# Performance work log

Hardware: AMD Instinct MI355X
Metric: run time of the kernel (lower is better)

Reference implementation:

```python
import jax, jax.numpy as jnp
import numpy as np

B = 4096      # batch of states
N = 32        # SVGD particles per state
D_ACT = 16    # action dim
D_OBS = 64    # obs dim
H = 256       # critic hidden width
STEPS = 3     # num_svgd_steps
LR = 0.1      # svgd_lr
LIMIT = 1.0   # act_limit


def q_mlp(obs, x, w1, b1, w2, b2, w3, b3):
    # SAC-style critic: q(obs, a) -> scalar per row. obs/x: [BN, *]
    h = jnp.concatenate([obs, x], axis=-1)
    h = jax.nn.relu(h @ w1 + b1)
    h = jax.nn.relu(h @ w2 + b2)
    return (h @ w3 + b3)[..., 0]  # [BN]


def rbf_kernel(X, Y):
    # X: [B, N, D] (differentiable), Y: [B, N, D] (detached copy of X)
    diff = X[:, :, None, :] - Y[:, None, :, :]          # [B, N, N, D]
    dist_sq = jnp.sum(diff * diff, axis=-1)             # [B, N, N]
    # median heuristic bandwidth per batch element
    med = jnp.median(dist_sq.reshape(dist_sq.shape[0], -1), axis=-1)
    h = med / np.log(N) + 1e-8
    gamma = jax.lax.stop_gradient(1.0 / (2.0 * h))      # [B]
    K = jnp.exp(-gamma[:, None, None] * dist_sq)        # [B, N, N]
    # dK/dX (grad wrt first argument)
    K_grad = -2.0 * gamma[:, None, None, None] * diff * K[..., None]  # [B,N,N,D]
    return K, diff, gamma, K_grad


def setup_inputs() -> dict:
    key = jax.random.key(0)
    ks = jax.random.split(key, 6)
    BN = B * N
    sc = lambda k, shp: jax.random.normal(k, shp, jnp.float32) * 0.05
    return {
        "obs": jax.random.normal(ks[0], (BN, D_OBS), jnp.float32),
        "a": jax.random.normal(ks[1], (BN, D_ACT), jnp.float32),
        "w1": sc(ks[2], (D_OBS + D_ACT, H)),
        "b1": jnp.zeros((H,), jnp.float32),
        "w2": sc(ks[3], (H, H)),
        "b2": jnp.zeros((H,), jnp.float32),
        "w3": sc(ks[4], (H, 1)),
        "b3": jnp.zeros((1,), jnp.float32),
    }


def reference(obs, a, w1, b1, w2, b2, w3, b3):
    # a0 arrives detached in the original (sampler(obs, a0.detach(), ...))
    a = jax.lax.stop_gradient(a)
    logp = jnp.zeros((B, N), jnp.float32)
    q_fn = lambda X: q_mlp(obs, X, w1, b1, w2, b2, w3, b3)
    q_vals = None
    for _ in range(STEPS):
        # log_prob = min(q1, q1) == q1; score = d(sum q)/dX via vjp
        q_vals, vjp_fn = jax.vjp(q_fn, a)                 # q_vals: [BN]
        score, = vjp_fn(jnp.ones_like(q_vals))            # [BN, D_ACT]
        X = a.reshape(B, N, D_ACT)
        S = score.reshape(B, N, D_ACT)
        K, diff, gamma, K_grad = rbf_kernel(X, jax.lax.stop_gradient(X))
        # phi = (K.detach() @ score - K_grad.sum(2)) / N
        drive = jnp.einsum('bij,bjd->bid', jax.lax.stop_gradient(K), S)
        phi = (drive - K_grad.sum(axis=2)) / N            # [B, N, D]
        # logp correction terms
        tmp1 = (K_grad * S[:, None, :, :]).sum(-1).mean(-1)                 # [B, N]
        tmp2 = -2.0 * gamma[:, None] * (((-K_grad) * diff).sum(-1)
                                        - D_ACT * K).mean(-1)               # [B, N]
        logp = logp - LR * (tmp1 + tmp2)
        # svgd_optim + clamp + detach
        a = a + LR * phi.reshape(B * N, D_ACT)
        a = jax.lax.stop_gradient(jnp.clip(a, -LIMIT, LIMIT))
    return a.reshape(B, N, D_ACT), logp, q_vals
```

## Files before the change

kernel.cpp:

```cpp
#include <hip/hip_runtime.h>
#include <hip/hip_bf16.h>
#include <math.h>

#define BNROWS (4096*32)
#define RB     64
#define LN32   3.4657359027997265f

typedef __attribute__((ext_vector_type(8))) short bf16x8;
typedef __attribute__((ext_vector_type(4))) float f32x4;

static __device__ __forceinline__ ushort f2bf(float x) {
    union { __hip_bfloat16 h; ushort u; } cv;
    cv.h = __float2bfloat16(x);
    return cv.u;
}

__global__ void obs_to_bf16(const float* __restrict__ obs,
                            ushort* __restrict__ obs_bf) {
    size_t i = ((size_t)blockIdx.x * 256 + threadIdx.x) * 4;
    float4 v = *(const float4*)&obs[i];
    ushort4 o;
    o.x = f2bf(v.x); o.y = f2bf(v.y); o.z = f2bf(v.z); o.w = f2bf(v.w);
    *(ushort4*)&obs_bf[i] = o;
}

__global__ void prep_pack(const float* __restrict__ w1,
                          const float* __restrict__ w2,
                          ushort* __restrict__ pB1, ushort* __restrict__ pB2,
                          ushort* __restrict__ pB3, ushort* __restrict__ pB4) {
    int g = blockIdx.x * 256 + threadIdx.x;
    ushort out[8];
    ushort* dst;
    if (g < 3072) {
        int lane = g & 63, gc = g >> 6;
        int t = gc / 3, c = gc % 3;
        int m = lane & 15, q = lane >> 4, n = t * 16 + m;
        #pragma unroll
        for (int j = 0; j < 8; ++j) {
            int k = c * 32 + q * 8 + j;
            out[j] = f2bf((k < 80) ? w1[k * 256 + n] : 0.f);
        }
        dst = &pB1[g * 8];
    } else if (g < 11264) {
        int gg = g - 3072;
        int lane = gg & 63, gc = gg >> 6;
        int t = gc >> 3, c = gc & 7;
        int m = lane & 15, q = lane >> 4, n = t * 16 + m;
        #pragma unroll
        for (int j = 0; j < 8; ++j)
            out[j] = f2bf(w2[(c * 32 + q * 8 + j) * 256 + n]);
        dst = &pB2[gg * 8];
    } else if (g < 19456) {
        int gg = g - 11264;
        int lane = gg & 63, gc = gg >> 6;
        int t = gc >> 3, c = gc & 7;
        int m = lane & 15, q = lane >> 4;
        #pragma unroll
        for (int j = 0; j < 8; ++j)
            out[j] = f2bf(w2[(t * 16 + m) * 256 + c * 32 + q * 8 + j]);
        dst = &pB3[gg * 8];
    } else if (g < 19968) {
        int gg = g - 19456;
        int lane = gg & 63, c = gg >> 6;
        int m = lane & 15, q = lane >> 4;
        #pragma unroll
        for (int j = 0; j < 8; ++j)
            out[j] = f2bf(w1[(64 + m) * 256 + c * 32 + q * 8 + j]);
        dst = &pB4[gg * 8];
    } else return;
    *(uint4*)dst = *(uint4*)out;
}

__global__ __launch_bounds__(512) void mlp_mfma(
    const ushort* __restrict__ obs_bf,
    const float* __restrict__ a_in,
    const float* __restrict__ b1,
    const float* __restrict__ b2,
    const float* __restrict__ w3,
    const float* __restrict__ b3,
    const ushort* __restrict__ pB1, const ushort* __restrict__ pB2,
    const ushort* __restrict__ pB3, const ushort* __restrict__ pB4,
    float* __restrict__ score,
    float* __restrict__ qout)
{
    __shared__ __align__(16) ushort B0[RB * 264];
    __shared__ __align__(16) ushort B1s[RB * 104];
    __shared__ float qpart[8][RB];
    __shared__ float bias1[256], bias2[256], w3s[256];

    const int tid  = threadIdx.x;
    const int row0 = blockIdx.x * RB;

    {
        int r = tid >> 3, ch = tid & 7;
        *(uint4*)&B1s[r * 104 + ch * 8] =
            *(const uint4*)&obs_bf[(size_t)(row0 + r) * 64 + ch * 8];
    }
    if (tid < 256) {
        int r = tid >> 2, d0 = (tid & 3) * 4;
        float4 av = *(const float4*)&a_in[(size_t)(row0 + r) * 16 + d0];
        ushort4 pv;
        pv.x = f2bf(av.x); pv.y = f2bf(av.y); pv.z = f2bf(av.z); pv.w = f2bf(av.w);
        *(ushort4*)&B1s[r * 104 + 64 + d0] = pv;
        ushort4 zv; zv.x = zv.y = zv.z = zv.w = 0;
        *(ushort4*)&B1s[r * 104 + 80 + d0] = zv;
        bias1[tid] = b1[tid]; bias2[tid] = b2[tid]; w3s[tid] = w3[tid];
    }
    __syncthreads();

    const int lane = tid & 63;
    const int w    = tid >> 6;
    const int m    = lane & 15;
    const int q    = lane >> 4;
    const int qk   = q * 8;

    f32x4 acc[4][2];
    unsigned relumask = 0u;

    #pragma unroll
    for (int tc = 0; tc < 2; ++tc)
        #pragma unroll
        for (int rt = 0; rt < 4; ++rt) acc[rt][tc] = (f32x4){0.f, 0.f, 0.f, 0.f};
    for (int c = 0; c < 3; ++c) {
        bf16x8 af[4];
        #pragma unroll
        for (int rt = 0; rt < 4; ++rt)
            af[rt] = *(const bf16x8*)&B1s[(rt * 16 + m) * 104 + c * 32 + qk];
        #pragma unroll
        for (int tc = 0; tc < 2; ++tc) {
            bf16x8 wfr = *(const bf16x8*)&pB1[(((w * 2 + tc) * 3 + c) * 64 + lane) * 8];
            #pragma unroll
            for (int rt = 0; rt < 4; ++rt)
                acc[rt][tc] = __builtin_amdgcn_mfma_f32_16x16x32_bf16(wfr, af[rt], acc[rt][tc], 0, 0, 0);
        }
    }
    #pragma unroll
    for (int tc = 0; tc < 2; ++tc) {
        const float4 bv = *(const float4*)&bias1[(w * 2 + tc) * 16 + q * 4];
        const float bva[4] = {bv.x, bv.y, bv.z, bv.w};
        #pragma unroll
        for (int rt = 0; rt < 4; ++rt) {
            ushort4 pk;
            float z0 = acc[rt][tc][0] + bva[0];
            float z1 = acc[rt][tc][1] + bva[1];
            float z2 = acc[rt][tc][2] + bva[2];
            float z3 = acc[rt][tc][3] + bva[3];
            if (z0 > 0.f) relumask |= 1u << (rt * 8 + tc * 4 + 0);
            if (z1 > 0.f) relumask |= 1u << (rt * 8 + tc * 4 + 1);
            if (z2 > 0.f) relumask |= 1u << (rt * 8 + tc * 4 + 2);
            if (z3 > 0.f) relumask |= 1u << (rt * 8 + tc * 4 + 3);
            pk.x = f2bf(fmaxf(z0, 0.f)); pk.y = f2bf(fmaxf(z1, 0.f));
            pk.z = f2bf(fmaxf(z2, 0.f)); pk.w = f2bf(fmaxf(z3, 0.f));
            *(ushort4*)&B0[(rt * 16 + m) * 264 + (w * 2 + tc) * 16 + q * 4] = pk;
        }
    }
    __syncthreads();

    #pragma unroll
    for (int tc = 0; tc < 2; ++tc)
        #pragma unroll
        for (int rt = 0; rt < 4; ++rt) acc[rt][tc] = (f32x4){0.f, 0.f, 0.f, 0.f};
    for (int c = 0; c < 8; ++c) {
        bf16x8 af[4];
        #pragma unroll
        for (int rt = 0; rt < 4; ++rt)
            af[rt] = *(const bf16x8*)&B0[(rt * 16 + m) * 264 + c * 32 + qk];
        #pragma unroll
        for (int tc = 0; tc < 2; ++tc) {
            bf16x8 wfr = *(const bf16x8*)&pB2[(((w * 2 + tc) * 8 + c) * 64 + lane) * 8];
            #pragma unroll
            for (int rt = 0; rt < 4; ++rt)
                acc[rt][tc] = __builtin_amdgcn_mfma_f32_16x16x32_bf16(wfr, af[rt], acc[rt][tc], 0, 0, 0);
        }
    }
    __syncthreads();
    {
        float qp[4] = {0.f, 0.f, 0.f, 0.f};
        #pragma unroll
        for (int tc = 0; tc < 2; ++tc) {
            const float4 bv = *(const float4*)&bias2[(w * 2 + tc) * 16 + q * 4];
            const float4 wv = *(const float4*)&w3s[(w * 2 + tc) * 16 + q * 4];
            const float bva[4] = {bv.x, bv.y, bv.z, bv.w};
            const float wva[4] = {wv.x, wv.y, wv.z, wv.w};
            #pragma unroll
            for (int rt = 0; rt < 4; ++rt) {
                ushort4 pk; float dz[4];
                #pragma unroll
                for (int i = 0; i < 4; ++i) {
                    float z = acc[rt][tc][i] + bva[i];
                    if (z > 0.f) { qp[rt] += z * wva[i]; dz[i] = wva[i]; }
                    else         { dz[i] = 0.f; }
                }
                pk.x = f2bf(dz[0]); pk.y = f2bf(dz[1]);
                pk.z = f2bf(dz[2]); pk.w = f2bf(dz[3]);
                *(ushort4*)&B0[(rt * 16 + m) * 264 + (w * 2 + tc) * 16 + q * 4] = pk;
            }
        }
        #pragma unroll
        for (int rt = 0; rt < 4; ++rt) {
            float v = qp[rt];
            v += __shfl_xor(v, 16); v += __shfl_xor(v, 32);
            if (q == 0) qpart[w][rt * 16 + m] = v;
        }
    }
    __syncthreads();

    if (tid < RB) {
        float qs = b3[0];
        #pragma unroll
        for (int ww = 0; ww < 8; ++ww) qs += qpart[ww][tid];
        qout[row0 + tid] = qs;
    }

    #pragma unroll
    for (int tc = 0; tc < 2; ++tc)
        #pragma unroll
        for (int rt = 0; rt < 4; ++rt) acc[rt][tc] = (f32x4){0.f, 0.f, 0.f, 0.f};
    for (int c = 0; c < 8; ++c) {
        bf16x8 af[4];
        #pragma unroll
        for (int rt = 0; rt < 4; ++rt)
            af[rt] = *(const bf16x8*)&B0[(rt * 16 + m) * 264 + c * 32 + qk];
        #pragma unroll
        for (int tc = 0; tc < 2; ++tc) {
            bf16x8 wfr = *(const bf16x8*)&pB3[(((w * 2 + tc) * 8 + c) * 64 + lane) * 8];
            #pragma unroll
            for (int rt = 0; rt < 4; ++rt)
                acc[rt][tc] = __builtin_amdgcn_mfma_f32_16x16x32_bf16(wfr, af[rt], acc[rt][tc], 0, 0, 0);
        }
    }
    __syncthreads();
    #pragma unroll
    for (int rt = 0; rt < 4; ++rt)
        #pragma unroll
        for (int tc = 0; tc < 2; ++tc) {
            ushort4 pk;
            pk.x = f2bf((relumask >> (rt * 8 + tc * 4 + 0)) & 1u ? acc[rt][tc][0] : 0.f);
            pk.y = f2bf((relumask >> (rt * 8 + tc * 4 + 1)) & 1u ? acc[rt][tc][1] : 0.f);
            pk.z = f2bf((relumask >> (rt * 8 + tc * 4 + 2)) & 1u ? acc[rt][tc][2] : 0.f);
            pk.w = f2bf((relumask >> (rt * 8 + tc * 4 + 3)) & 1u ? acc[rt][tc][3] : 0.f);
            *(ushort4*)&B0[(rt * 16 + m) * 264 + (w * 2 + tc) * 16 + q * 4] = pk;
        }
    __syncthreads();

    if (w < 4) {
        f32x4 acc2 = (f32x4){0.f, 0.f, 0.f, 0.f};
        for (int c = 0; c < 8; ++c) {
            bf16x8 af = *(const bf16x8*)&B0[(w * 16 + m) * 264 + c * 32 + qk];
            bf16x8 wfr = *(const bf16x8*)&pB4[(c * 64 + lane) * 8];
            acc2 = __builtin_amdgcn_mfma_f32_16x16x32_bf16(wfr, af, acc2, 0, 0, 0);
        }
        float4 o; o.x = acc2[0]; o.y = acc2[1]; o.z = acc2[2]; o.w = acc2[3];
        *(float4*)&score[(size_t)(row0 + w * 16 + m) * 16 + q * 4] = o;
    }
}

__global__ __launch_bounds__(256, 4) void svgd_kernel(
    const float* __restrict__ a_in,
    const float* __restrict__ score,
    const float* __restrict__ logp_in,
    float* __restrict__ logp_out,
    float* __restrict__ a_out,
    int first)
{
    __shared__ float X[32 * 17], S[32 * 17];
    __shared__ float KM[32 * 40];
    __shared__ int hist[2048];
    __shared__ int wsum[4];
    __shared__ int bbin, bexcl;
    __shared__ int redc[4];
    __shared__ unsigned redm[4];

    const int b = blockIdx.x, tid = threadIdx.x;
    const int lane = tid & 63, wv = tid >> 6;
    const size_t base = (size_t)b * 512;

    for (int idx = tid; idx < 512; idx += 256) {
        int r = idx >> 4, d = idx & 15;
        X[r * 17 + d] = a_in[base + idx];
        S[r * 17 + d] = score[base + idx];
    }
    __syncthreads();

    unsigned v[4]; float p[4];
    #pragma unroll
    for (int t = 0; t < 4; ++t) {
        int idx = tid + 256 * t, i = idx >> 5, j = idx & 31;
        float s = 0.f, pp = 0.f;
        #pragma unroll
        for (int d = 0; d < 16; ++d) {
            float df = X[i * 17 + d] - X[j * 17 + d];
            s  = fmaf(df, df, s);
            pp = fmaf(df, S[j * 17 + d], pp);
        }
        v[t] = __float_as_uint(s);
        p[t] = pp;
    }

    unsigned prefix = 0;
    int rank = 511;
    #pragma unroll
    for (int pass = 0; pass < 3; ++pass) {
        const int sh = (pass == 0) ? 21 : (pass == 1) ? 10 : 0;
        const unsigned dmask = (pass == 2) ? 1023u : 2047u;
        #pragma unroll
        for (int k = 0; k < 8; ++k) hist[tid + 256 * k] = 0;
        __syncthreads();
        #pragma unroll
        for (int t = 0; t < 4; ++t) {
            bool ok = (pass == 0) ||
                      ((v[t] >> (sh + ((pass == 1) ? 11 : 10))) == prefix);
            if (ok) atomicAdd(&hist[(v[t] >> sh) & dmask], 1);
        }
        __syncthreads();
        int c[8], ct = 0;
        #pragma unroll
        for (int k = 0; k < 8; ++k) { c[k] = hist[8 * tid + k]; ct += c[k]; }
        int inc = ct;
        #pragma unroll
        for (int off = 1; off < 64; off <<= 1) {
            int tt = __shfl_up(inc, off, 64);
            if (lane >= off) inc += tt;
        }
        if (lane == 63) wsum[wv] = inc;
        __syncthreads();
        int run = inc - ct;
        for (int ww = 0; ww < wv; ++ww) run += wsum[ww];
        #pragma unroll
        for (int k = 0; k < 8; ++k) {
            if (c[k] > 0 && rank >= run && rank < run + c[k]) {
                bbin = 8 * tid + k; bexcl = run;
            }
            run += c[k];
        }
        __syncthreads();
        prefix = (prefix << ((pass == 2) ? 10 : 11)) | (unsigned)bbin;
        rank -= bexcl;
    }
    const float v1 = __uint_as_float(prefix);

    float med;
    {
        int cle = 0;
        unsigned mgt = 0xFFFFFFFFu;
        #pragma unroll
        for (int t = 0; t < 4; ++t) {
            if (v[t] <= prefix) cle++;
            else mgt = min(mgt, v[t]);
        }
        #pragma unroll
        for (int off = 1; off < 64; off <<= 1) {
            cle += __shfl_xor(cle, off);
            mgt = min(mgt, (unsigned)__shfl_xor((int)mgt, off));
        }
        if (lane == 0) { redc[wv] = cle; redm[wv] = mgt; }
        __syncthreads();
        int C = redc[0] + redc[1] + redc[2] + redc[3];
        unsigned M = min(min(redm[0], redm[1]), min(redm[2], redm[3]));
        float v2 = (C >= 513) ? v1 : __uint_as_float(M);
        med = 0.5f * (v1 + v2);
    }
    const float gamma = 1.0f / (2.0f * (med / LN32 + 1e-8f));

    float kreg[4];
    #pragma unroll
    for (int t = 0; t < 4; ++t) {
        int idx = tid + 256 * t, i = idx >> 5, j = idx & 31;
        float kk = __expf(-gamma * __uint_as_float(v[t]));
        kreg[t] = kk;
        KM[i * 40 + j] = kk;
    }

    {
        float acc1[4], acc2[4];
        #pragma unroll
        for (int t = 0; t < 4; ++t) {
            float a1 = kreg[t] * p[t];
            float a2 = (2.f * gamma * __uint_as_float(v[t]) - 16.f) * kreg[t];
            #pragma unroll
            for (int off = 1; off < 32; off <<= 1) {
                a1 += __shfl_xor(a1, off);
                a2 += __shfl_xor(a2, off);
            }
            acc1[t] = a1; acc2[t] = a2;
        }
        if ((tid & 31) == 0) {
            #pragma unroll
            for (int t = 0; t < 4; ++t) {
                int i = (tid >> 5) + 8 * t;
                float tmp = -2.f * gamma * (acc1[t] + acc2[t]) * (1.f / 32.f);
                float prev = first ? 0.f : logp_in[b * 32 + i];
                logp_out[b * 32 + i] = prev - 0.1f * tmp;
            }
        }
    }
    __syncthreads();

    for (int idx = tid; idx < 512; idx += 256) {
        int i = idx >> 4, d = idx & 15;
        float s1 = 0.f, s2 = 0.f;
        float xi = X[i * 17 + d];
        #pragma unroll
        for (int j = 0; j < 32; ++j) {
            float kk = KM[i * 40 + j];
            s1 = fmaf(kk, S[j * 17 + d], s1);
            s2 = fmaf(kk, xi - X[j * 17 + d], s2);
        }
        float phi = (s1 + 2.f * gamma * s2) * (1.f / 32.f);
        float av = xi + 0.1f * phi;
        av = fminf(fmaxf(av, -1.f), 1.f);
        a_out[base + idx] = av;
    }
}

extern "C" void kernel_launch(void* const* d_in, const int* in_sizes, int n_in,
                              void* d_out, int out_size, void* d_ws, size_t ws_size,
                              hipStream_t stream) {
    const float* obs = (const float*)d_in[0];
    const float* a0  = (const float*)d_in[1];
    const float* w1  = (const float*)d_in[2];
    const float* b1  = (const float*)d_in[3];
    const float* w2  = (const float*)d_in[4];
    const float* b2  = (const float*)d_in[5];
    const float* w3  = (const float*)d_in[6];
    const float* b3  = (const float*)d_in[7];

    float* out_a    = (float*)d_out;
    float* out_logp = out_a + (size_t)BNROWS * 16;
    float* out_q    = out_logp + BNROWS;

    char* p = (char*)d_ws;
    ushort* pB1 = (ushort*)p; p += 24576 * 2;
    ushort* pB2 = (ushort*)p; p += 65536 * 2;
    ushort* pB3 = (ushort*)p; p += 65536 * 2;
    ushort* pB4 = (ushort*)p; p += 4096 * 2;
    ushort* obs_bf = (ushort*)p; p += (size_t)BNROWS * 64 * 2;
    float* abuf0 = (float*)p; p += (size_t)BNROWS * 16 * 4;
    float* abuf1 = (float*)p; p += (size_t)BNROWS * 16 * 4;
    float* scr   = (float*)p; p += (size_t)BNROWS * 16 * 4;
    float* logp  = (float*)p; p += (size_t)BNROWS * 4;
    float* qtmp  = (float*)p;

    prep_pack<<<78, 256, 0, stream>>>(w1, w2, pB1, pB2, pB3, pB4);
    obs_to_bf16<<<8192, 256, 0, stream>>>(obs, obs_bf);

    const int MB = BNROWS / RB;

    mlp_mfma<<<MB, 512, 0, stream>>>(obs_bf, a0, b1, b2, w3, b3,
                                     pB1, pB2, pB3, pB4, scr, qtmp);
    svgd_kernel<<<4096, 256, 0, stream>>>(a0, scr, nullptr, logp, abuf0, 1);
    mlp_mfma<<<MB, 512, 0, stream>>>(obs_bf, abuf0, b1, b2, w3, b3,
                                     pB1, pB2, pB3, pB4, scr, qtmp);
    svgd_kernel<<<4096, 256, 0, stream>>>(abuf0, scr, logp, logp, abuf1, 0);
    mlp_mfma<<<MB, 512, 0, stream>>>(obs_bf, abuf1, b1, b2, w3, b3,
                                     pB1, pB2, pB3, pB4, scr, out_q);
    svgd_kernel<<<4096, 256, 0, stream>>>(abuf1, scr, logp, out_logp, out_a, 0);
}
```

Before: 381.5 us.

## Fuse all SVGD steps and MLP into one persistent per-block kernel

Replaces the six alternating MLP and SVGD launches, plus the obs conversion kernel, with a single kernel. Each 64-row block holds two full particle sets, runs the MLP forward and backward for the score, computes the RBF kernel and median via a packed two-set radix histogram, and updates actions in shared memory across all three steps. This removes global round trips for score, actions and logp, and the launch gaps between steps. In exchange, obs is converted to bf16 inline in the kernel, q is accumulated with atomics, and the shared-memory reuse of B0 for the SVGD scratch raises LDS pressure and serializes the SVGD phase with the MFMA work inside each block.

```diff
diff --git a/kernel.cpp b/kernel.cpp
--- a/kernel.cpp
+++ b/kernel.cpp
@@ -13,15 +13,6 @@
     union { __hip_bfloat16 h; ushort u; } cv;
     cv.h = __float2bfloat16(x);
     return cv.u;
-}
-
-__global__ void obs_to_bf16(const float* __restrict__ obs,
-                            ushort* __restrict__ obs_bf) {
-    size_t i = ((size_t)blockIdx.x * 256 + threadIdx.x) * 4;
-    float4 v = *(const float4*)&obs[i];
-    ushort4 o;
-    o.x = f2bf(v.x); o.y = f2bf(v.y); o.z = f2bf(v.z); o.w = f2bf(v.w);
-    *(ushort4*)&obs_bf[i] = o;
 }
 
 __global__ void prep_pack(const float* __restrict__ w1,
@@ -71,8 +62,8 @@
     *(uint4*)dst = *(uint4*)out;
 }
 
-__global__ __launch_bounds__(512) void mlp_mfma(
-    const ushort* __restrict__ obs_bf,
+__global__ __launch_bounds__(512) void fused_svgd(
+    const float* __restrict__ obs,
     const float* __restrict__ a_in,
     const float* __restrict__ b1,
     const float* __restrict__ b2,
@@ -80,32 +71,50 @@
     const float* __restrict__ b3,
     const ushort* __restrict__ pB1, const ushort* __restrict__ pB2,
     const ushort* __restrict__ pB3, const ushort* __restrict__ pB4,
-    float* __restrict__ score,
+    float* __restrict__ a_out,
+    float* __restrict__ logp_out,
     float* __restrict__ qout)
 {
     __shared__ __align__(16) ushort B0[RB * 264];
     __shared__ __align__(16) ushort B1s[RB * 104];
-    __shared__ float qpart[8][RB];
+    __shared__ __align__(16) float  Xs[RB * 17];
     __shared__ float bias1[256], bias2[256], w3s[256];
+
+    float*    const Sv     = (float*)B0;
+    float*    const KM     = (float*)B0 + 1088;
+    int*      const hist   = (int*)B0 + 3648;
+    int*      const wsum   = (int*)B0 + 5696;
+    int*      const redc   = (int*)B0 + 5704;
+    unsigned* const redm   = (unsigned*)B0 + 5712;
+    int*      const bbin2  = (int*)B0 + 5720;
+    int*      const bexcl2 = (int*)B0 + 5722;
+    float*    const gamma2 = (float*)B0 + 5724;
 
     const int tid  = threadIdx.x;
     const int row0 = blockIdx.x * RB;
 
     {
         int r = tid >> 3, ch = tid & 7;
-        *(uint4*)&B1s[r * 104 + ch * 8] =
-            *(const uint4*)&obs_bf[(size_t)(row0 + r) * 64 + ch * 8];
+        const float* op = &obs[(size_t)(row0 + r) * 64 + ch * 8];
+        float4 v0 = *(const float4*)op;
+        float4 v1 = *(const float4*)(op + 4);
+        ushort o[8];
+        o[0] = f2bf(v0.x); o[1] = f2bf(v0.y); o[2] = f2bf(v0.z); o[3] = f2bf(v0.w);
+        o[4] = f2bf(v1.x); o[5] = f2bf(v1.y); o[6] = f2bf(v1.z); o[7] = f2bf(v1.w);
+        *(uint4*)&B1s[r * 104 + ch * 8] = *(uint4*)o;
+    }
+    #pragma unroll
+    for (int u = 0; u < 2; ++u) {
+        int idx = tid + 512 * u;
+        Xs[(idx >> 4) * 17 + (idx & 15)] = a_in[(size_t)row0 * 16 + idx];
     }
     if (tid < 256) {
         int r = tid >> 2, d0 = (tid & 3) * 4;
-        float4 av = *(const float4*)&a_in[(size_t)(row0 + r) * 16 + d0];
-        ushort4 pv;
-        pv.x = f2bf(av.x); pv.y = f2bf(av.y); pv.z = f2bf(av.z); pv.w = f2bf(av.w);
-        *(ushort4*)&B1s[r * 104 + 64 + d0] = pv;
         ushort4 zv; zv.x = zv.y = zv.z = zv.w = 0;
         *(ushort4*)&B1s[r * 104 + 80 + d0] = zv;
         bias1[tid] = b1[tid]; bias2[tid] = b2[tid]; w3s[tid] = w3[tid];
     }
+    if (tid < 64) qout[row0 + tid] = b3[0];
     __syncthreads();
 
     const int lane = tid & 63;
@@ -113,303 +122,310 @@
     const int m    = lane & 15;
     const int q    = lane >> 4;
     const int qk   = q * 8;
-
-    f32x4 acc[4][2];
-    unsigned relumask = 0u;
-
-    #pragma unroll
-    for (int tc = 0; tc < 2; ++tc)
-        #pragma unroll
-        for (int rt = 0; rt < 4; ++rt) acc[rt][tc] = (f32x4){0.f, 0.f, 0.f, 0.f};
-    for (int c = 0; c < 3; ++c) {
-        bf16x8 af[4];
+    const int st   = tid >> 8;
+    const int t8   = tid & 255;
+    const int wv4  = w & 3;
+
+    float lgp[4] = {0.f, 0.f, 0.f, 0.f};
+
+    #pragma unroll 1
+    for (int s = 0; s < 3; ++s) {
+        {
+            int r = tid >> 3, cp = (tid & 7) * 2;
+            ushort2 pv;
+            pv.x = f2bf(Xs[r * 17 + cp]);
+            pv.y = f2bf(Xs[r * 17 + cp + 1]);
+            *(ushort2*)&B1s[r * 104 + 64 + cp] = pv;
+        }
+        __syncthreads();
+
+        f32x4 acc[4][2];
+        unsigned relumask = 0u;
+
+        #pragma unroll
+        for (int tc = 0; tc < 2; ++tc)
+            #pragma unroll
+            for (int rt = 0; rt < 4; ++rt) acc[rt][tc] = (f32x4){0.f, 0.f, 0.f, 0.f};
+        for (int c = 0; c < 3; ++c) {
+            bf16x8 af[4];
+            #pragma unroll
+            for (int rt = 0; rt < 4; ++rt)
+                af[rt] = *(const bf16x8*)&B1s[(rt * 16 + m) * 104 + c * 32 + qk];
+            #pragma unroll
+            for (int tc = 0; tc < 2; ++tc) {
+                bf16x8 wfr = *(const bf16x8*)&pB1[(((w * 2 + tc) * 3 + c) * 64 + lane) * 8];
+                #pragma unroll
+                for (int rt = 0; rt < 4; ++rt)
+                    acc[rt][tc] = __builtin_amdgcn_mfma_f32_16x16x32_bf16(wfr, af[rt], acc[rt][tc], 0, 0, 0);
+            }
+        }
+        #pragma unroll
+        for (int tc = 0; tc < 2; ++tc) {
+            const float4 bv = *(const float4*)&bias1[(w * 2 + tc) * 16 + q * 4];
+            const float bva[4] = {bv.x, bv.y, bv.z, bv.w};
+            #pragma unroll
+            for (int rt = 0; rt < 4; ++rt) {
+                ushort4 pk;
+                float z0 = acc[rt][tc][0] + bva[0];
+                float z1 = acc[rt][tc][1] + bva[1];
+                float z2 = acc[rt][tc][2] + bva[2];
+                float z3 = acc[rt][tc][3] + bva[3];
+                if (z0 > 0.f) relumask |= 1u << (rt * 8 + tc * 4 + 0);
+                if (z1 > 0.f) relumask |= 1u << (rt * 8 + tc * 4 + 1);
+                if (z2 > 0.f) relumask |= 1u << (rt * 8 + tc * 4 + 2);
+                if (z3 > 0.f) relumask |= 1u << (rt * 8 + tc * 4 + 3);
+                pk.x = f2bf(fmaxf(z0, 0.f)); pk.y = f2bf(fmaxf(z1, 0.f));
+                pk.z = f2bf(fmaxf(z2, 0.f)); pk.w = f2bf(fmaxf(z3, 0.f));
+                *(ushort4*)&B0[(rt * 16 + m) * 264 + (w * 2 + tc) * 16 + q * 4] = pk;
+            }
+        }
+        __syncthreads();
+
+        #pragma unroll
+        for (int tc = 0; tc < 2; ++tc)
+            #pragma unroll
+            for (int rt = 0; rt < 4; ++rt) acc[rt][tc] = (f32x4){0.f, 0.f, 0.f, 0.f};
+        for (int c = 0; c < 8; ++c) {
+            bf16x8 af[4];
+            #pragma unroll
+            for (int rt = 0; rt < 4; ++rt)
+                af[rt] = *(const bf16x8*)&B0[(rt * 16 + m) * 264 + c * 32 + qk];
+            #pragma unroll
+            for (int tc = 0; tc < 2; ++tc) {
+                bf16x8 wfr = *(const bf16x8*)&pB2[(((w * 2 + tc) * 8 + c) * 64 + lane) * 8];
+                #pragma unroll
+                for (int rt = 0; rt < 4; ++rt)
+                    acc[rt][tc] = __builtin_amdgcn_mfma_f32_16x16x32_bf16(wfr, af[rt], acc[rt][tc], 0, 0, 0);
+            }
+        }
+        __syncthreads();
+        {
+            float qp[4] = {0.f, 0.f, 0.f, 0.f};
+            #pragma unroll
+            for (int tc = 0; tc < 2; ++tc) {
+                const float4 bv = *(const float4*)&bias2[(w * 2 + tc) * 16 + q * 4];
+                const float4 wv = *(const float4*)&w3s[(w * 2 + tc) * 16 + q * 4];
+                const float bva[4] = {bv.x, bv.y, bv.z, bv.w};
+                const float wva[4] = {wv.x, wv.y, wv.z, wv.w};
+                #pragma unroll
+                for (int rt = 0; rt < 4; ++rt) {
+                    ushort4 pk; float dz[4];
+                    #pragma unroll
+                    for (int i = 0; i < 4; ++i) {
+                        float z = acc[rt][tc][i] + bva[i];
+                        if (z > 0.f) { qp[rt] += z * wva[i]; dz[i] = wva[i]; }
+                        else         { dz[i] = 0.f; }
+                    }
+                    pk.x = f2bf(dz[0]); pk.y = f2bf(dz[1]);
+                    pk.z = f2bf(dz[2]); pk.w = f2bf(dz[3]);
+                    *(ushort4*)&B0[(rt * 16 + m) * 264 + (w * 2 + tc) * 16 + q * 4] = pk;
+                }
+            }
+            if (s == 2) {
+                #pragma unroll
+                for (int rt = 0; rt < 4; ++rt) {
+                    float v = qp[rt];
+                    v += __shfl_xor(v, 16); v += __shfl_xor(v, 32);
+                    if (q == 0) atomicAdd(&qout[row0 + rt * 16 + m], v);
+                }
+            }
+        }
+        __syncthreads();
+
+        #pragma unroll
+        for (int tc = 0; tc < 2; ++tc)
+            #pragma unroll
+            for (int rt = 0; rt < 4; ++rt) acc[rt][tc] = (f32x4){0.f, 0.f, 0.f, 0.f};
+        for (int c = 0; c < 8; ++c) {
+            bf16x8 af[4];
+            #pragma unroll
+            for (int rt = 0; rt < 4; ++rt)
+                af[rt] = *(const bf16x8*)&B0[(rt * 16 + m) * 264 + c * 32 + qk];
+            #pragma unroll
+            for (int tc = 0; tc < 2; ++tc) {
+                bf16x8 wfr = *(const bf16x8*)&pB3[(((w * 2 + tc) * 8 + c) * 64 + lane) * 8];
+                #pragma unroll
+                for (int rt = 0; rt < 4; ++rt)
+                    acc[rt][tc] = __builtin_amdgcn_mfma_f32_16x16x32_bf16(wfr, af[rt], acc[rt][tc], 0, 0, 0);
+            }
+        }
+        __syncthreads();
         #pragma unroll
         for (int rt = 0; rt < 4; ++rt)
-            af[rt] = *(const bf16x8*)&B1s[(rt * 16 + m) * 104 + c * 32 + qk];
-        #pragma unroll
-        for (int tc = 0; tc < 2; ++tc) {
-            bf16x8 wfr = *(const bf16x8*)&pB1[(((w * 2 + tc) * 3 + c) * 64 + lane) * 8];
-            #pragma unroll
-            for (int rt = 0; rt < 4; ++rt)
-                acc[rt][tc] = __builtin_amdgcn_mfma_f32_16x16x32_bf16(wfr, af[rt], acc[rt][tc], 0, 0, 0);
-        }
-    }
-    #pragma unroll
-    for (int tc = 0; tc < 2; ++tc) {
-        const float4 bv = *(const float4*)&bias1[(w * 2 + tc) * 16 + q * 4];
-        const float bva[4] = {bv.x, bv.y, bv.z, bv.w};
-        #pragma unroll
-        for (int rt = 0; rt < 4; ++rt) {
-            ushort4 pk;
-            float z0 = acc[rt][tc][0] + bva[0];
-            float z1 = acc[rt][tc][1] + bva[1];
-            float z2 = acc[rt][tc][2] + bva[2];
-            float z3 = acc[rt][tc][3] + bva[3];
-            if (z0 > 0.f) relumask |= 1u << (rt * 8 + tc * 4 + 0);
-            if (z1 > 0.f) relumask |= 1u << (rt * 8 + tc * 4 + 1);
-            if (z2 > 0.f) relumask |= 1u << (rt * 8 + tc * 4 + 2);
-            if (z3 > 0.f) relumask |= 1u << (rt * 8 + tc * 4 + 3);
-            pk.x = f2bf(fmaxf(z0, 0.f)); pk.y = f2bf(fmaxf(z1, 0.f));
-            pk.z = f2bf(fmaxf(z2, 0.f)); pk.w = f2bf(fmaxf(z3, 0.f));
-            *(ushort4*)&B0[(rt * 16 + m) * 264 + (w * 2 + tc) * 16 + q * 4] = pk;
-        }
-    }
-    __syncthreads();
-
-    #pragma unroll
-    for (int tc = 0; tc < 2; ++tc)
-        #pragma unroll
-        for (int rt = 0; rt < 4; ++rt) acc[rt][tc] = (f32x4){0.f, 0.f, 0.f, 0.f};
-    for (int c = 0; c < 8; ++c) {
-        bf16x8 af[4];
-        #pragma unroll
-        for (int rt = 0; rt < 4; ++rt)
-            af[rt] = *(const bf16x8*)&B0[(rt * 16 + m) * 264 + c * 32 + qk];
-        #pragma unroll
-        for (int tc = 0; tc < 2; ++tc) {
-            bf16x8 wfr = *(const bf16x8*)&pB2[(((w * 2 + tc) * 8 + c) * 64 + lane) * 8];
-            #pragma unroll
-            for (int rt = 0; rt < 4; ++rt)
-                acc[rt][tc] = __builtin_amdgcn_mfma_f32_16x16x32_bf16(wfr, af[rt], acc[rt][tc], 0, 0, 0);
-        }
-    }
-    __syncthreads();
-    {
-        float qp[4] = {0.f, 0.f, 0.f, 0.f};
-        #pragma unroll
-        for (int tc = 0; tc < 2; ++tc) {
-            const float4 bv = *(const float4*)&bias2[(w * 2 + tc) * 16 + q * 4];
-            const float4 wv = *(const float4*)&w3s[(w * 2 + tc) * 16 + q * 4];
-            const float bva[4] = {bv.x, bv.y, bv.z, bv.w};
-            const float wva[4] = {wv.x, wv.y, wv.z, wv.w};
-            #pragma unroll
-            for (int rt = 0; rt < 4; ++rt) {
-                ushort4 pk; float dz[4];
-                #pragma unroll
-                for (int i = 0; i < 4; ++i) {
-                    float z = acc[rt][tc][i] + bva[i];
-                    if (z > 0.f) { qp[rt] += z * wva[i]; dz[i] = wva[i]; }
-                    else         { dz[i] = 0.f; }
+            #pragma unroll
+            for (int tc = 0; tc < 2; ++tc) {
+                ushort4 pk;
+                pk.x = f2bf((relumask >> (rt * 8 + tc * 4 + 0)) & 1u ? acc[rt][tc][0] : 0.f);
+                pk.y = f2bf((relumask >> (rt * 8 + tc * 4 + 1)) & 1u ? acc[rt][tc][1] : 0.f);
+                pk.z = f2bf((relumask >> (rt * 8 + tc * 4 + 2)) & 1u ? acc[rt][tc][2] : 0.f);
+                pk.w = f2bf((relumask >> (rt * 8 + tc * 4 + 3)) & 1u ? acc[rt][tc][3] : 0.f);
+                *(ushort4*)&B0[(rt * 16 + m) * 264 + (w * 2 + tc) * 16 + q * 4] = pk;
+            }
+        __syncthreads();
+
+        f32x4 accE = (f32x4){0.f, 0.f, 0.f, 0.f};
+        if (w < 4) {
+            for (int c = 0; c < 8; ++c) {
+                bf16x8 af = *(const bf16x8*)&B0[(w * 16 + m) * 264 + c * 32 + qk];
+                bf16x8 wfr = *(const bf16x8*)&pB4[(c * 64 + lane) * 8];
+                accE = __builtin_amdgcn_mfma_f32_16x16x32_bf16(wfr, af, accE, 0, 0, 0);
+            }
+        }
+        __syncthreads();
+        if (w < 4) {
+            float* Sr = &Sv[(w * 16 + m) * 17 + q * 4];
+            Sr[0] = accE[0]; Sr[1] = accE[1]; Sr[2] = accE[2]; Sr[3] = accE[3];
+        }
+        __syncthreads();
+
+        unsigned vb[4]; float pr[4];
+        #pragma unroll
+        for (int t = 0; t < 4; ++t) {
+            int idx = t8 + 256 * t, i = idx >> 5, j = idx & 31;
+            int gi = st * 32 + i, gj = st * 32 + j;
+            float ss = 0.f, pp = 0.f;
+            #pragma unroll
+            for (int d = 0; d < 16; ++d) {
+                float df = Xs[gi * 17 + d] - Xs[gj * 17 + d];
+                ss = fmaf(df, df, ss);
+                pp = fmaf(df, Sv[gj * 17 + d], pp);
+            }
+            vb[t] = __float_as_uint(ss);
+            pr[t] = pp;
+        }
+
+        unsigned prefix = 0;
+        int rank = 511;
+        const int addv = 1 << (st * 16);
+        #pragma unroll 1
+        for (int pass = 0; pass < 3; ++pass) {
+            const int sh = (pass == 0) ? 21 : (pass == 1) ? 10 : 0;
+            const unsigned dmask = (pass == 2) ? 1023u : 2047u;
+            #pragma unroll
+            for (int k = 0; k < 4; ++k) hist[tid + 512 * k] = 0;
+            __syncthreads();
+            #pragma unroll
+            for (int t = 0; t < 4; ++t) {
+                bool ok = (pass == 0) ||
+                          ((vb[t] >> (sh + ((pass == 1) ? 11 : 10))) == prefix);
+                if (ok) atomicAdd(&hist[(vb[t] >> sh) & dmask], addv);
+            }
+            __syncthreads();
+            int c[8], ct = 0;
+            #pragma unroll
+            for (int k = 0; k < 8; ++k) {
+                c[k] = (hist[8 * t8 + k] >> (st * 16)) & 0xFFFF;
+                ct += c[k];
+            }
+            int inc = ct;
+            #pragma unroll
+            for (int off = 1; off < 64; off <<= 1) {
+                int tt = __shfl_up(inc, off, 64);
+                if (lane >= off) inc += tt;
+            }
+            if (lane == 63) wsum[st * 4 + wv4] = inc;
+            __syncthreads();
+            int run = inc - ct;
+            for (int ww = 0; ww < wv4; ++ww) run += wsum[st * 4 + ww];
+            #pragma unroll
+            for (int k = 0; k < 8; ++k) {
+                if (c[k] > 0 && rank >= run && rank < run + c[k]) {
+                    bbin2[st] = 8 * t8 + k; bexcl2[st] = run;
                 }
-                pk.x = f2bf(dz[0]); pk.y = f2bf(dz[1]);
-                pk.z = f2bf(dz[2]); pk.w = f2bf(dz[3]);
-                *(ushort4*)&B0[(rt * 16 + m) * 264 + (w * 2 + tc) * 16 + q * 4] = pk;
-            }
-        }
-        #pragma unroll
-        for (int rt = 0; rt < 4; ++rt) {
-            float v = qp[rt];
-            v += __shfl_xor(v, 16); v += __shfl_xor(v, 32);
-            if (q == 0) qpart[w][rt * 16 + m] = v;
-        }
-    }
-    __syncthreads();
-
-    if (tid < RB) {
-        float qs = b3[0];
-        #pragma unroll
-        for (int ww = 0; ww < 8; ++ww) qs += qpart[ww][tid];
-        qout[row0 + tid] = qs;
-    }
-
-    #pragma unroll
-    for (int tc = 0; tc < 2; ++tc)
-        #pragma unroll
-        for (int rt = 0; rt < 4; ++rt) acc[rt][tc] = (f32x4){0.f, 0.f, 0.f, 0.f};
-    for (int c = 0; c < 8; ++c) {
-        bf16x8 af[4];
-        #pragma unroll
-        for (int rt = 0; rt < 4; ++rt)
-            af[rt] = *(const bf16x8*)&B0[(rt * 16 + m) * 264 + c * 32 + qk];
-        #pragma unroll
-        for (int tc = 0; tc < 2; ++tc) {
-            bf16x8 wfr = *(const bf16x8*)&pB3[(((w * 2 + tc) * 8 + c) * 64 + lane) * 8];
-            #pragma unroll
-            for (int rt = 0; rt < 4; ++rt)
-                acc[rt][tc] = __builtin_amdgcn_mfma_f32_16x16x32_bf16(wfr, af[rt], acc[rt][tc], 0, 0, 0);
-        }
-    }
-    __syncthreads();
-    #pragma unroll
-    for (int rt = 0; rt < 4; ++rt)
-        #pragma unroll
-        for (int tc = 0; tc < 2; ++tc) {
-            ushort4 pk;
-            pk.x = f2bf((relumask >> (rt * 8 + tc * 4 + 0)) & 1u ? acc[rt][tc][0] : 0.f);
-            pk.y = f2bf((relumask >> (rt * 8 + tc * 4 + 1)) & 1u ? acc[rt][tc][1] : 0.f);
-            pk.z = f2bf((relumask >> (rt * 8 + tc * 4 + 2)) & 1u ? acc[rt][tc][2] : 0.f);
-            pk.w = f2bf((relumask >> (rt * 8 + tc * 4 + 3)) & 1u ? acc[rt][tc][3] : 0.f);
-            *(ushort4*)&B0[(rt * 16 + m) * 264 + (w * 2 + tc) * 16 + q * 4] = pk;
-        }
-    __syncthreads();
-
-    if (w < 4) {
-        f32x4 acc2 = (f32x4){0.f, 0.f, 0.f, 0.f};
-        for (int c = 0; c < 8; ++c) {
-            bf16x8 af = *(const bf16x8*)&B0[(w * 16 + m) * 264 + c * 32 + qk];
-            bf16x8 wfr = *(const bf16x8*)&pB4[(c * 64 + lane) * 8];
-            acc2 = __builtin_amdgcn_mfma_f32_16x16x32_bf16(wfr, af, acc2, 0, 0, 0);
-        }
-        float4 o; o.x = acc2[0]; o.y = acc2[1]; o.z = acc2[2]; o.w = acc2[3];
-        *(float4*)&score[(size_t)(row0 + w * 16 + m) * 16 + q * 4] = o;
-    }
-}
-
-__global__ __launch_bounds__(256, 4) void svgd_kernel(
-    const float* __restrict__ a_in,
-    const float* __restrict__ score,
-    const float* __restrict__ logp_in,
-    float* __restrict__ logp_out,
-    float* __restrict__ a_out,
-    int first)
-{
-    __shared__ float X[32 * 17], S[32 * 17];
-    __shared__ float KM[32 * 40];
-    __shared__ int hist[2048];
-    __shared__ int wsum[4];
-    __shared__ int bbin, bexcl;
-    __shared__ int redc[4];
-    __shared__ unsigned redm[4];
-
-    const int b = blockIdx.x, tid = threadIdx.x;
-    const int lane = tid & 63, wv = tid >> 6;
-    const size_t base = (size_t)b * 512;
-
-    for (int idx = tid; idx < 512; idx += 256) {
-        int r = idx >> 4, d = idx & 15;
-        X[r * 17 + d] = a_in[base + idx];
-        S[r * 17 + d] = score[base + idx];
-    }
-    __syncthreads();
-
-    unsigned v[4]; float p[4];
-    #pragma unroll
-    for (int t = 0; t < 4; ++t) {
-        int idx = tid + 256 * t, i = idx >> 5, j = idx & 31;
-        float s = 0.f, pp = 0.f;
-        #pragma unroll
-        for (int d = 0; d < 16; ++d) {
-            float df = X[i * 17 + d] - X[j * 17 + d];
-            s  = fmaf(df, df, s);
-            pp = fmaf(df, S[j * 17 + d], pp);
-        }
-        v[t] = __float_as_uint(s);
-        p[t] = pp;
-    }
-
-    unsigned prefix = 0;
-    int rank = 511;
-    #pragma unroll
-    for (int pass = 0; pass < 3; ++pass) {
-        const int sh = (pass == 0) ? 21 : (pass == 1) ? 10 : 0;
-        const unsigned dmask = (pass == 2) ? 1023u : 2047u;
-        #pragma unroll
-        for (int k = 0; k < 8; ++k) hist[tid + 256 * k] = 0;
-        __syncthreads();
+                run += c[k];
+            }
+            __syncthreads();
+            prefix = (prefix << ((pass == 2) ? 10 : 11)) | (unsigned)bbin2[st];
+            rank -= bexcl2[st];
+        }
+        const float v1 = __uint_as_float(prefix);
+
+        float med;
+        {
+            int cle = 0;
+            unsigned mgt = 0xFFFFFFFFu;
+            #pragma unroll
+            for (int t = 0; t < 4; ++t) {
+                if (vb[t] <= prefix) cle++;
+                else mgt = min(mgt, vb[t]);
+            }
+            #pragma unroll
+            for (int off = 1; off < 64; off <<= 1) {
+                cle += __shfl_xor(cle, off);
+                mgt = min(mgt, (unsigned)__shfl_xor((int)mgt, off));
+            }
+            if (lane == 0) { redc[st * 4 + wv4] = cle; redm[st * 4 + wv4] = mgt; }
+            __syncthreads();
+            int C = redc[st * 4 + 0] + redc[st * 4 + 1] + redc[st * 4 + 2] + redc[st * 4 + 3];
+            unsigned M = min(min(redm[st * 4 + 0], redm[st * 4 + 1]),
+                             min(redm[st * 4 + 2], redm[st * 4 + 3]));
+            float v2 = (C >= 513) ? v1 : __uint_as_float(M);
+            med = 0.5f * (v1 + v2);
+        }
+        const float gamma = 1.0f / (2.0f * (med / LN32 + 1e-8f));
+        if (t8 == 0) gamma2[st] = gamma;
+
+        float kreg[4];
         #pragma unroll
         for (int t = 0; t < 4; ++t) {
-            bool ok = (pass == 0) ||
-                      ((v[t] >> (sh + ((pass == 1) ? 11 : 10))) == prefix);
-            if (ok) atomicAdd(&hist[(v[t] >> sh) & dmask], 1);
-        }
-        __syncthreads();
-        int c[8], ct = 0;
-        #pragma unroll
-        for (int k = 0; k < 8; ++k) { c[k] = hist[8 * tid + k]; ct += c[k]; }
-        int inc = ct;
-        #pragma unroll
-        for (int off = 1; off < 64; off <<= 1) {
-            int tt = __shfl_up(inc, off, 64);
-            if (lane >= off) inc += tt;
-        }
-        if (lane == 63) wsum[wv] = inc;
-        __syncthreads();
-        int run = inc - ct;
-        for (int ww = 0; ww < wv; ++ww) run += wsum[ww];
-        #pragma unroll
-        for (int k = 0; k < 8; ++k) {
-            if (c[k] > 0 && rank >= run && rank < run + c[k]) {
-                bbin = 8 * tid + k; bexcl = run;
-            }
-            run += c[k];
-        }
-        __syncthreads();
-        prefix = (prefix << ((pass == 2) ? 10 : 11)) | (unsigned)bbin;
-        rank -= bexcl;
-    }
-    const float v1 = __uint_as_float(prefix);
-
-    float med;
-    {
-        int cle = 0;
-        unsigned mgt = 0xFFFFFFFFu;
-        #pragma unroll
-        for (int t = 0; t < 4; ++t) {
-            if (v[t] <= prefix) cle++;
-            else mgt = min(mgt, v[t]);
-        }
-        #pragma unroll
-        for (int off = 1; off < 64; off <<= 1) {
-            cle += __shfl_xor(cle, off);
-            mgt = min(mgt, (unsigned)__shfl_xor((int)mgt, off));
-        }
-        if (lane == 0) { redc[wv] = cle; redm[wv] = mgt; }
-        __syncthreads();
-        int C = redc[0] + redc[1] + redc[2] + redc[3];
-        unsigned M = min(min(redm[0], redm[1]), min(redm[2], redm[3]));
-        float v2 = (C >= 513) ? v1 : __uint_as_float(M);
-        med = 0.5f * (v1 + v2);
-    }
-    const float gamma = 1.0f / (2.0f * (med / LN32 + 1e-8f));
-
-    float kreg[4];
-    #pragma unroll
-    for (int t = 0; t < 4; ++t) {
-        int idx = tid + 256 * t, i = idx >> 5, j = idx & 31;
-        float kk = __expf(-gamma * __uint_as_float(v[t]));
-        kreg[t] = kk;
-        KM[i * 40 + j] = kk;
-    }
-
-    {
-        float acc1[4], acc2[4];
-        #pragma unroll
-        for (int t = 0; t < 4; ++t) {
-            float a1 = kreg[t] * p[t];
-            float a2 = (2.f * gamma * __uint_as_float(v[t]) - 16.f) * kreg[t];
-            #pragma unroll
-            for (int off = 1; off < 32; off <<= 1) {
-                a1 += __shfl_xor(a1, off);
-                a2 += __shfl_xor(a2, off);
-            }
-            acc1[t] = a1; acc2[t] = a2;
-        }
-        if ((tid & 31) == 0) {
+            int idx = t8 + 256 * t, i = idx >> 5, j = idx & 31;
+            float kk = __expf(-gamma * __uint_as_float(vb[t]));
+            kreg[t] = kk;
+            KM[(st * 32 + i) * 40 + j] = kk;
+        }
+
+        {
+            float a1s[4], a2s[4];
             #pragma unroll
             for (int t = 0; t < 4; ++t) {
-                int i = (tid >> 5) + 8 * t;
-                float tmp = -2.f * gamma * (acc1[t] + acc2[t]) * (1.f / 32.f);
-                float prev = first ? 0.f : logp_in[b * 32 + i];
-                logp_out[b * 32 + i] = prev - 0.1f * tmp;
-            }
-        }
-    }
-    __syncthreads();
-
-    for (int idx = tid; idx < 512; idx += 256) {
-        int i = idx >> 4, d = idx & 15;
-        float s1 = 0.f, s2 = 0.f;
-        float xi = X[i * 17 + d];
-        #pragma unroll
-        for (int j = 0; j < 32; ++j) {
-            float kk = KM[i * 40 + j];
-            s1 = fmaf(kk, S[j * 17 + d], s1);
-            s2 = fmaf(kk, xi - X[j * 17 + d], s2);
-        }
-        float phi = (s1 + 2.f * gamma * s2) * (1.f / 32.f);
-        float av = xi + 0.1f * phi;
-        av = fminf(fmaxf(av, -1.f), 1.f);
-        a_out[base + idx] = av;
+                float a1 = kreg[t] * pr[t];
+                float a2 = (2.f * gamma * __uint_as_float(vb[t]) - 16.f) * kreg[t];
+                #pragma unroll
+                for (int off = 1; off < 32; off <<= 1) {
+                    a1 += __shfl_xor(a1, off);
+                    a2 += __shfl_xor(a2, off);
+                }
+                a1s[t] = a1; a2s[t] = a2;
+            }
+            if ((tid & 31) == 0) {
+                #pragma unroll
+                for (int t = 0; t < 4; ++t) {
+                    int i = (t8 >> 5) + 8 * t;
+                    float tmp = -2.f * gamma * (a1s[t] + a2s[t]) * (1.f / 32.f);
+                    lgp[t] -= 0.1f * tmp;
+                    if (s == 2) logp_out[row0 + st * 32 + i] = lgp[t];
+                }
+            }
+        }
+        __syncthreads();
+
+        float av[2];
+        #pragma unroll
+        for (int u = 0; u < 2; ++u) {
+            int idx = tid + 512 * u;
+            int i = idx >> 4, d = idx & 15;
+            int sb = (i >> 5) * 32;
+            float g = gamma2[i >> 5];
+            float xi = Xs[i * 17 + d];
+            float s1 = 0.f, s2 = 0.f;
+            #pragma unroll
+            for (int j = 0; j < 32; ++j) {
+                float kk = KM[i * 40 + j];
+                s1 = fmaf(kk, Sv[(sb + j) * 17 + d], s1);
+                s2 = fmaf(kk, xi - Xs[(sb + j) * 17 + d], s2);
+            }
+            float phi = (s1 + 2.f * g * s2) * (1.f / 32.f);
+            float t = xi + 0.1f * phi;
+            av[u] = fminf(fmaxf(t, -1.f), 1.f);
+        }
+        __syncthreads();
+        #pragma unroll
+        for (int u = 0; u < 2; ++u) {
+            int idx = tid + 512 * u;
+            Xs[(idx >> 4) * 17 + (idx & 15)] = av[u];
+            if (s == 2) a_out[(size_t)row0 * 16 + idx] = av[u];
+        }
+        __syncthreads();
     }
 }
 
@@ -433,26 +449,12 @@
     ushort* pB1 = (ushort*)p; p += 24576 * 2;
     ushort* pB2 = (ushort*)p; p += 65536 * 2;
     ushort* pB3 = (ushort*)p; p += 65536 * 2;
-    ushort* pB4 = (ushort*)p; p += 4096 * 2;
-    ushort* obs_bf = (ushort*)p; p += (size_t)BNROWS * 64 * 2;
-    float* abuf0 = (float*)p; p += (size_t)BNROWS * 16 * 4;
-    float* abuf1 = (float*)p; p += (size_t)BNROWS * 16 * 4;
-    float* scr   = (float*)p; p += (size_t)BNROWS * 16 * 4;
-    float* logp  = (float*)p; p += (size_t)BNROWS * 4;
-    float* qtmp  = (float*)p;
+    ushort* pB4 = (ushort*)p;
 
     prep_pack<<<78, 256, 0, stream>>>(w1, w2, pB1, pB2, pB3, pB4);
-    obs_to_bf16<<<8192, 256, 0, stream>>>(obs, obs_bf);
 
     const int MB = BNROWS / RB;
-
-    mlp_mfma<<<MB, 512, 0, stream>>>(obs_bf, a0, b1, b2, w3, b3,
-                                     pB1, pB2, pB3, pB4, scr, qtmp);
-    svgd_kernel<<<4096, 256, 0, stream>>>(a0, scr, nullptr, logp, abuf0, 1);
-    mlp_mfma<<<MB, 512, 0, stream>>>(obs_bf, abuf0, b1, b2, w3, b3,
-                                     pB1, pB2, pB3, pB4, scr, qtmp);
-    svgd_kernel<<<4096, 256, 0, stream>>>(abuf0, scr, logp, logp, abuf1, 0);
-    mlp_mfma<<<MB, 512, 0, stream>>>(obs_bf, abuf1, b1, b2, w3, b3,
-                                     pB1, pB2, pB3, pB4, scr, out_q);
-    svgd_kernel<<<4096, 256, 0, stream>>>(abuf1, scr, logp, out_logp, out_a, 0);
+    fused_svgd<<<MB, 512, 0, stream>>>(obs, a0, b1, b2, w3, b3,
+                                       pB1, pB2, pB3, pB4,
+                                       out_a, out_logp, out_q);
 }
```

New measurement: 659.6 us. +72.9%, slower.
